# Performance work log

Hardware: AMD Instinct MI355X
Metric: run time of the kernel (lower is better)

## Reference

```python
import jax, jax.numpy as jnp
import numpy as np

B, L, E, H, RR, BIO, NT, V, R = 16, 128, 256, 256, 128, 64, 3, 30000, 25


def setup_inputs() -> dict:
    key = jax.random.key(0)
    ks = jax.random.split(key, 24)
    s = 0.05
    n = jax.random.normal
    inp = {
        'tokens': jax.random.randint(ks[0], (B, L), 0, V),
        'bio_gold': jax.random.randint(ks[1], (B, L), 0, NT),
        'selection_gold': jax.random.uniform(ks[2], (B, L, R, L), jnp.float32),
        'word_emb': n(ks[3], (V, E), jnp.float32) * s,
        'W_ih_f': n(ks[4], (4 * H, E), jnp.float32) * s,
        'W_hh_f': n(ks[5], (4 * H, H), jnp.float32) * s,
        'b_f': n(ks[6], (4 * H,), jnp.float32) * s,
        'W_ih_b': n(ks[7], (4 * H, E), jnp.float32) * s,
        'W_hh_b': n(ks[8], (4 * H, H), jnp.float32) * s,
        'b_b': n(ks[9], (4 * H,), jnp.float32) * s,
        'emi_W': n(ks[10], (NT, H), jnp.float32) * s,
        'emi_b': n(ks[11], (NT,), jnp.float32) * s,
        'bio_emb': n(ks[12], (NT + 1, BIO), jnp.float32) * s,
        'sel_u_W': n(ks[13], (RR, H + BIO), jnp.float32) * s,
        'sel_u_b': n(ks[14], (RR,), jnp.float32) * s,
        'sel_v_W': n(ks[15], (RR, H + BIO), jnp.float32) * s,
        'sel_v_b': n(ks[16], (RR,), jnp.float32) * s,
        'sel_uv_W': n(ks[17], (RR, 2 * RR), jnp.float32) * s,
        'sel_uv_b': n(ks[18], (RR,), jnp.float32) * s,
        'rel_emb': n(ks[19], (R, RR), jnp.float32) * s,
        'crf_start': n(ks[20], (NT,), jnp.float32) * s,
        'crf_end': n(ks[21], (NT,), jnp.float32) * s,
        'crf_trans': n(ks[22], (NT, NT), jnp.float32) * s,
    }
    return inp


def _lstm(x, W_ih, W_hh, b, reverse):
    # x: [B,L,E] -> hidden states [B,L,H]; PyTorch gate order i,f,g,o
    Bb = x.shape[0]
    Hh = W_hh.shape[1]
    xg = jnp.swapaxes(jnp.einsum('ble,ge->blg', x, W_ih) + b, 0, 1)  # [L,B,4H]

    def step(carry, xt):
        h, c = carry
        g = xt + h @ W_hh.T
        i, f, gg, o = jnp.split(g, 4, axis=-1)
        c = jax.nn.sigmoid(f) * c + jax.nn.sigmoid(i) * jnp.tanh(gg)
        h = jax.nn.sigmoid(o) * jnp.tanh(c)
        return (h, c), h

    init = (jnp.zeros((Bb, Hh), x.dtype), jnp.zeros((Bb, Hh), x.dtype))
    _, hs = jax.lax.scan(step, init, xg, reverse=reverse)
    return jnp.swapaxes(hs, 0, 1)


def reference(tokens, bio_gold, selection_gold, word_emb, W_ih_f, W_hh_f, b_f,
              W_ih_b, W_hh_b, b_b, emi_W, emi_b, bio_emb, sel_u_W, sel_u_b,
              sel_v_W, sel_v_b, sel_uv_W, sel_uv_b, rel_emb, crf_start,
              crf_end, crf_trans):
    mask = tokens != 0  # pad id 0
    maskf = mask.astype(jnp.float32)
    emb = word_emb[tokens]
    # BiLSTM, halves averaged as in (fwd + bwd) / 2
    o = (_lstm(emb, W_ih_f, W_hh_f, b_f, False)
         + _lstm(emb, W_ih_b, W_hh_b, b_b, True)) * 0.5
    emi = o @ emi_W.T + emi_b  # [B,L,NT]

    # ---- CRF negative log-likelihood (torchcrf, reduction='mean') ----
    bidx = jnp.arange(tokens.shape[0])
    e_sel = jnp.take_along_axis(emi, bio_gold[..., None], axis=2)[..., 0]  # [B,L]
    num = crf_start[bio_gold[:, 0]] + e_sel[:, 0]
    tr = crf_trans[bio_gold[:, :-1], bio_gold[:, 1:]]  # [B,L-1]
    num = num + ((tr + e_sel[:, 1:]) * maskf[:, 1:]).sum(1)
    seq_ends = jnp.maximum(mask.sum(1) - 1, 0)
    num = num + crf_end[bio_gold[bidx, seq_ends]]

    def crf_step(score, inp):
        emi_t, m_t = inp
        nxt = jax.nn.logsumexp(score[:, :, None] + crf_trans[None] + emi_t[:, None, :], axis=1)
        return jnp.where(m_t[:, None], nxt, score), None

    score0 = crf_start + emi[:, 0]
    score, _ = jax.lax.scan(crf_step, score0,
                            (jnp.swapaxes(emi[:, 1:], 0, 1), jnp.swapaxes(mask[:, 1:], 0, 1)))
    den = jax.nn.logsumexp(score + crf_end, axis=1)
    crf_loss = -(num - den).mean()

    # ---- pairwise biaffine selection head ----
    oc = jnp.concatenate([o, bio_emb[bio_gold]], axis=-1)  # [B,L,H+BIO]
    u = jax.nn.relu(oc @ sel_u_W.T + sel_u_b)  # [B,L,RR]
    v = jax.nn.relu(oc @ sel_v_W.T + sel_v_b)
    Rr = rel_emb.shape[1]
    W1, W2 = sel_uv_W[:, :Rr], sel_uv_W[:, Rr:]  # split cat([u,v]) linear
    a = u @ W1.T  # indexed by j (u was expanded along dim 1)
    c = v @ W2.T  # indexed by i
    uv = jax.nn.relu(a[:, None, :, :] + c[:, :, None, :] + sel_uv_b)  # [B,L,L,RR]
    logits = jnp.einsum('bijh,rh->birj', uv, rel_emb)  # [B,L,R,L]

    y = selection_gold
    bce = jnp.maximum(logits, 0) - logits * y + jnp.log1p(jnp.exp(-jnp.abs(logits)))
    selmask = maskf[:, :, None, None] * maskf[:, None, None, :]  # [B,L,1,L]
    sel_loss = (bce * selmask).sum() / maskf.sum()
    return crf_loss + sel_loss
```

## Files before the change

kernel.cpp:

```cpp
#include <hip/hip_runtime.h>
#include <cstdint>
#include <cstddef>


typedef __attribute__((ext_vector_type(8))) short short8;
typedef __attribute__((ext_vector_type(8))) int i32x8;
typedef __attribute__((ext_vector_type(4))) float f32x4;

__device__ __forceinline__ unsigned short f2bf(float f) {
  unsigned int u = __float_as_uint(f);
  u += 0x7fffu + ((u >> 16) & 1u);
  return (unsigned short)(u >> 16);
}
__device__ __forceinline__ float bf2f(unsigned short u) {
  return __uint_as_float(((unsigned int)u) << 16);
}

__device__ __forceinline__ void dev_pp8k128(const float* __restrict__ W,
                                            unsigned int* __restrict__ out, int idx) {
  int c = idx & 3;
  int lane = (idx >> 2) & 63;
  int f = idx >> 8;
  int nt = f >> 1, kt = f & 1;
  int n = nt * 16 + (lane & 15);
  int k0 = kt * 128 + (lane >> 4) * 32 + c * 8;
  const float* wp = &W[(size_t)n * 256 + k0];
  int lo = 0, hi = 0;
  lo = __builtin_amdgcn_cvt_pk_fp8_f32(wp[0], wp[1], lo, false);
  lo = __builtin_amdgcn_cvt_pk_fp8_f32(wp[2], wp[3], lo, true);
  hi = __builtin_amdgcn_cvt_pk_fp8_f32(wp[4], wp[5], hi, false);
  hi = __builtin_amdgcn_cvt_pk_fp8_f32(wp[6], wp[7], hi, true);
  size_t base = ((size_t)(f << 6) + lane) * 8 + (c << 1);
  out[base] = (unsigned)lo;
  out[base + 1] = (unsigned)hi;
}

__device__ __forceinline__ void dev_ppw(const float* __restrict__ W, int ldw, int nkt,
                                        uint4* __restrict__ out, int idx) {
  int lane = idx & 63;
  int f = idx >> 6;
  int kt = f % nkt;
  int nt = f / nkt;
  int row = nt * 16 + (lane & 15);
  int k0 = kt * 32 + ((lane >> 4) << 3);
  const float* wp = &W[(size_t)row * ldw + k0];
  union { unsigned short us[8]; uint4 v; } tmp;
#pragma unroll
  for (int j = 0; j < 8; ++j) tmp.us[j] = f2bf(wp[j]);
  out[idx] = tmp.v;
}

__global__ __launch_bounds__(256) void k_setup(
    const float* __restrict__ Whhf, unsigned int* __restrict__ wpk8f,
    const float* __restrict__ Whhb, unsigned int* __restrict__ wpk8b,
    const float* __restrict__ Wihf, uint4* __restrict__ wihfPk,
    const float* __restrict__ Wihb, uint4* __restrict__ wihbPk,
    const float* __restrict__ suW, uint4* __restrict__ suPk,
    const float* __restrict__ svW, uint4* __restrict__ svPk,
    const float* __restrict__ suvW, uint4* __restrict__ w1Pk, uint4* __restrict__ w2Pk,
    float* __restrict__ acc) {
  int bid = blockIdx.x;
  int t = threadIdx.x;
  if (bid < 128) {
    dev_pp8k128(Whhf, wpk8f, bid * 256 + t);
  } else if (bid < 256) {
    dev_pp8k128(Whhb, wpk8b, (bid - 128) * 256 + t);
  } else if (bid < 384) {
    dev_ppw(Wihf, 256, 8, wihfPk, (bid - 256) * 256 + t);
  } else if (bid < 512) {
    dev_ppw(Wihb, 256, 8, wihbPk, (bid - 384) * 256 + t);
  } else if (bid < 532) {
    dev_ppw(suW, 320, 10, suPk, (bid - 512) * 256 + t);
  } else if (bid < 552) {
    dev_ppw(svW, 320, 10, svPk, (bid - 532) * 256 + t);
  } else if (bid < 560) {
    dev_ppw(suvW, 256, 4, w1Pk, (bid - 552) * 256 + t);
  } else if (bid < 568) {
    dev_ppw(suvW + 128, 256, 4, w2Pk, (bid - 560) * 256 + t);
  } else {
    if (t < 16) acc[t] = 0.f;
  }
}

__global__ __launch_bounds__(256) void k_xg(
    const int* __restrict__ tok, const float* __restrict__ wemb,
    const uint4* __restrict__ WpkF, const float* __restrict__ biasF,
    unsigned short* __restrict__ PF,
    const uint4* __restrict__ WpkB, const float* __restrict__ biasB,
    unsigned short* __restrict__ PB) {
  const uint4* Wp = blockIdx.z ? WpkB : WpkF;
  const float* bi = blockIdx.z ? biasB : biasF;
  unsigned short* Po = blockIdx.z ? PB : PF;
  int bn = blockIdx.x, bm = blockIdx.y;
  int tid = threadIdx.x;
  int w = tid >> 6;
  int lane = tid & 63;
  int m = lane & 15;
  int q = lane >> 4;
  int arow = bm * 64 + w * 16 + m;
  const float* ew = wemb + (size_t)tok[arow] * 256 + (q << 3);
  f32x4 z = {0.f, 0.f, 0.f, 0.f};
  f32x4 ac[4] = {z, z, z, z};
  for (int kt = 0; kt < 8; ++kt) {
    float4 e0 = *reinterpret_cast<const float4*>(ew + (kt << 5));
    float4 e1 = *reinterpret_cast<const float4*>(ew + (kt << 5) + 4);
    union { unsigned short us[8]; short8 v; } af;
    af.us[0] = f2bf(e0.x); af.us[1] = f2bf(e0.y); af.us[2] = f2bf(e0.z); af.us[3] = f2bf(e0.w);
    af.us[4] = f2bf(e1.x); af.us[5] = f2bf(e1.y); af.us[6] = f2bf(e1.z); af.us[7] = f2bf(e1.w);
#pragma unroll
    for (int nt = 0; nt < 4; ++nt) {
      uint4 b4 = Wp[(size_t)(((bn << 2) + nt) * 8 + kt) * 64 + lane];
      ac[nt] = __builtin_amdgcn_mfma_f32_16x16x32_bf16(af.v, __builtin_bit_cast(short8, b4), ac[nt], 0, 0, 0);
    }
  }
#pragma unroll
  for (int nt = 0; nt < 4; ++nt) {
    int col = (bn << 6) + (nt << 4) + m;
    float bv = bi[col];
    int g = col >> 8;
    int cell = col & 255;
    int wl = cell >> 5;
    int nn = (cell >> 4) & 1;
    int mm = cell & 15;
#pragma unroll
    for (int reg = 0; reg < 4; ++reg) {
      int row = (bm << 6) + (w << 4) + (q << 2) + reg;
      int b = row >> 7;
      int t = row & 127;
      size_t pidx = ((size_t)b << 17) +
                    (size_t)(((t << 7) + (wl << 4) + mm) << 3) + (g << 1) + nn;
      Po[pidx] = f2bf(ac[nt][reg] + bv);
    }
  }
}

__global__ __launch_bounds__(512, 2) void k_lstm(
    const unsigned short* __restrict__ Pf, const unsigned short* __restrict__ Pb,
    const unsigned int* __restrict__ wpkf, const unsigned int* __restrict__ wpkb,
    unsigned short* __restrict__ hsf, unsigned short* __restrict__ hsb) {
  int bid = blockIdx.x;
  int dir = bid >> 4;
  int b = bid & 15;
  const unsigned short* P = (dir ? Pb : Pf) + ((size_t)b << 17);
  const unsigned int* wpk = dir ? wpkb : wpkf;
  unsigned short* hseq = (dir ? hsb : hsf) + (size_t)b * 128 * 256;

  __shared__ __align__(16) unsigned char h8[2][272];

  int tid = threadIdx.x;
  int w = tid >> 6;
  int lane = tid & 63;
  int m = lane & 15;
  int q = lane >> 4;
  int j0 = (w << 5) + m;

  i32x8 wfr[4][2][2];
#pragma unroll
  for (int g = 0; g < 4; ++g)
#pragma unroll
    for (int n = 0; n < 2; ++n)
#pragma unroll
      for (int kt = 0; kt < 2; ++kt) {
        int f = (((g << 4) + (w << 1) + n) << 1) + kt;
        wfr[g][n][kt] = *reinterpret_cast<const i32x8*>(wpk + (((size_t)(f << 6) + lane) << 3));
      }
#pragma unroll
  for (int g = 0; g < 4; ++g)
#pragma unroll
    for (int n = 0; n < 2; ++n)
#pragma unroll
      for (int kt = 0; kt < 2; ++kt)
        asm volatile("" : "+v"(wfr[g][n][kt]));

  if (tid < 136) reinterpret_cast<unsigned int*>(&h8[0][0])[tid] = 0u;
  __syncthreads();

  const f32x4 zero4 = {0.f, 0.f, 0.f, 0.f};
  float cst[2] = {0.f, 0.f};

  auto load_x = [&](int s) -> uint4 {
    int t = dir ? (127 - (s & 127)) : (s & 127);
    return *reinterpret_cast<const uint4*>(
        P + ((size_t)((t << 7) + (w << 4) + m) << 3));
  };

  auto step = [&](int s, uint4 x4) {
    int t = dir ? (127 - s) : s;
    const unsigned char* cur = &h8[s & 1][0];
    unsigned char* nxt = &h8[(s & 1) ^ 1][0];

    i32x8 afr[2];
#pragma unroll
    for (int kt = 0; kt < 2; ++kt) {
      union { uint4 u[2]; i32x8 v; } tmp;
      const unsigned char* hp = cur + kt * 128 + q * 32;
      tmp.u[0] = *reinterpret_cast<const uint4*>(hp);
      tmp.u[1] = *reinterpret_cast<const uint4*>(hp + 16);
      afr[kt] = tmp.v;
    }

    f32x4 acg[4][2];
    __builtin_amdgcn_s_setprio(1);
#pragma unroll
    for (int n = 0; n < 2; ++n) {
#pragma unroll
      for (int g = 0; g < 4; ++g)
        acg[g][n] = __builtin_amdgcn_mfma_scale_f32_16x16x128_f8f6f4(
            afr[0], wfr[g][n][0], zero4, 0, 0, 0, 0x7f7f7f7f, 0, 0x7f7f7f7f);
#pragma unroll
      for (int g = 0; g < 4; ++g)
        acg[g][n] = __builtin_amdgcn_mfma_scale_f32_16x16x128_f8f6f4(
            afr[1], wfr[g][n][1], acg[g][n], 0, 0, 0, 0x7f7f7f7f, 0, 0x7f7f7f7f);
    }
    __builtin_amdgcn_s_setprio(0);

    if (q == 0) {
      unsigned ug[4] = {x4.x, x4.y, x4.z, x4.w};
#pragma unroll
      for (int n = 0; n < 2; ++n) {
        float x0 = n ? __uint_as_float(ug[0] & 0xffff0000u) : __uint_as_float(ug[0] << 16);
        float x1 = n ? __uint_as_float(ug[1] & 0xffff0000u) : __uint_as_float(ug[1] << 16);
        float x2 = n ? __uint_as_float(ug[2] & 0xffff0000u) : __uint_as_float(ug[2] << 16);
        float x3 = n ? __uint_as_float(ug[3] & 0xffff0000u) : __uint_as_float(ug[3] << 16);
        float gi = acg[0][n][0] + x0;
        float gf = acg[1][n][0] + x1;
        float gg = acg[2][n][0] + x2;
        float go = acg[3][n][0] + x3;
        float si = __fdividef(1.f, 1.f + __expf(-gi));
        float sf = __fdividef(1.f, 1.f + __expf(-gf));
        float so = __fdividef(1.f, 1.f + __expf(-go));
        float tg = 1.f - __fdividef(2.f, __expf(2.f * gg) + 1.f);
        float cc = sf * cst[n] + si * tg;
        cst[n] = cc;
        float th = 1.f - __fdividef(2.f, __expf(2.f * cc) + 1.f);
        float h = so * th;
        int j = j0 + (n << 4);
        hseq[(size_t)t * 256 + j] = f2bf(h);
        int pk = __builtin_amdgcn_cvt_pk_fp8_f32(h, h, 0, false);
        nxt[j] = (unsigned char)(pk & 0xff);
      }
    }
    asm volatile("s_waitcnt lgkmcnt(0)" ::: "memory");
    __builtin_amdgcn_s_barrier();
    asm volatile("" ::: "memory");
  };

  uint4 xA = load_x(0);
  for (int sp = 0; sp < 128; sp += 2) {
    uint4 xB = load_x(sp + 1);
    step(sp, xA);
    xA = load_x(sp + 2);
    step(sp + 1, xB);
  }
}

__global__ __launch_bounds__(256) void k_mid2(
    const unsigned short* __restrict__ hf16, const unsigned short* __restrict__ hb16,
    const int* __restrict__ bio, const float* __restrict__ bioE,
    const float* __restrict__ emiW, const float* __restrict__ emib,
    const uint4* __restrict__ suPk, const float* __restrict__ sub,
    const uint4* __restrict__ svPk, const float* __restrict__ svb,
    const uint4* __restrict__ w1Pk, const uint4* __restrict__ w2Pk,
    unsigned short* __restrict__ a16, unsigned short* __restrict__ c16,
    float* __restrict__ emi) {
  __shared__ __align__(16) unsigned short oc[16][328];
  __shared__ __align__(16) unsigned short ub[16][136];
  __shared__ __align__(16) unsigned short vb[16][136];
  int r0 = blockIdx.x * 16;
  int tid = threadIdx.x;

#pragma unroll
  for (int it = 0; it < 8; ++it) {
    int i = it * 256 + tid;
    int row = i >> 7, h2 = (i & 127) << 1;
    unsigned int af = *reinterpret_cast<const unsigned int*>(hf16 + (size_t)(r0 + row) * 256 + h2);
    unsigned int ab = *reinterpret_cast<const unsigned int*>(hb16 + (size_t)(r0 + row) * 256 + h2);
    float lo = 0.5f * (bf2f((unsigned short)af) + bf2f((unsigned short)ab));
    float hi = 0.5f * (bf2f((unsigned short)(af >> 16)) + bf2f((unsigned short)(ab >> 16)));
    unsigned int pk = (unsigned int)f2bf(lo) | ((unsigned int)f2bf(hi) << 16);
    *reinterpret_cast<unsigned int*>(&oc[row][h2]) = pk;
  }
#pragma unroll
  for (int it = 0; it < 2; ++it) {
    int i = it * 256 + tid;
    int row = i >> 5, p = (i & 31) << 1;
    int bi = bio[r0 + row];
    float b0 = bioE[bi * 64 + p], b1 = bioE[bi * 64 + p + 1];
    unsigned int pk = (unsigned int)f2bf(b0) | ((unsigned int)f2bf(b1) << 16);
    *reinterpret_cast<unsigned int*>(&oc[row][256 + p]) = pk;
  }
  __syncthreads();

  if (tid < 192) {
    int did = tid >> 2, sub4 = tid & 3;
    int row = did / 3, g = did - row * 3;
    const float* ew = emiW + g * 256 + sub4 * 64;
    float av = 0.f;
#pragma unroll
    for (int k = 0; k < 64; ++k) av += bf2f(oc[row][sub4 * 64 + k]) * ew[k];
    av += __shfl_xor(av, 1);
    av += __shfl_xor(av, 2);
    if (sub4 == 0) emi[(size_t)(r0 + row) * 3 + g] = av + emib[g];
  }

  int w = tid >> 6, lane = tid & 63, m = lane & 15, q = lane >> 4;
  {
    f32x4 z = {0.f, 0.f, 0.f, 0.f};
    f32x4 au[2] = {z, z}, av2[2] = {z, z};
    for (int kt = 0; kt < 10; ++kt) {
      uint4 a4 = *reinterpret_cast<const uint4*>(&oc[m][(kt << 5) + (q << 3)]);
      short8 af = __builtin_bit_cast(short8, a4);
#pragma unroll
      for (int d = 0; d < 2; ++d) {
        int nt = (w << 1) + d;
        uint4 bu = suPk[(size_t)(nt * 10 + kt) * 64 + lane];
        uint4 bv = svPk[(size_t)(nt * 10 + kt) * 64 + lane];
        au[d] = __builtin_amdgcn_mfma_f32_16x16x32_bf16(af, __builtin_bit_cast(short8, bu), au[d], 0, 0, 0);
        av2[d] = __builtin_amdgcn_mfma_f32_16x16x32_bf16(af, __builtin_bit_cast(short8, bv), av2[d], 0, 0, 0);
      }
    }
#pragma unroll
    for (int d = 0; d < 2; ++d) {
      int col = ((w << 1) + d) * 16 + m;
      float bu = sub[col], bv = svb[col];
#pragma unroll
      for (int reg = 0; reg < 4; ++reg) {
        int row = (q << 2) + reg;
        ub[row][col] = f2bf(fmaxf(au[d][reg] + bu, 0.f));
        vb[row][col] = f2bf(fmaxf(av2[d][reg] + bv, 0.f));
      }
    }
  }
  __syncthreads();

  {
    f32x4 z = {0.f, 0.f, 0.f, 0.f};
    f32x4 aa[2] = {z, z}, cc[2] = {z, z};
    for (int kt = 0; kt < 4; ++kt) {
      uint4 ua = *reinterpret_cast<const uint4*>(&ub[m][(kt << 5) + (q << 3)]);
      uint4 va = *reinterpret_cast<const uint4*>(&vb[m][(kt << 5) + (q << 3)]);
      short8 uf = __builtin_bit_cast(short8, ua);
      short8 vf = __builtin_bit_cast(short8, va);
#pragma unroll
      for (int d = 0; d < 2; ++d) {
        int nt = (w << 1) + d;
        uint4 b1 = w1Pk[(size_t)((nt << 2) + kt) * 64 + lane];
        uint4 b2 = w2Pk[(size_t)((nt << 2) + kt) * 64 + lane];
        aa[d] = __builtin_amdgcn_mfma_f32_16x16x32_bf16(uf, __builtin_bit_cast(short8, b1), aa[d], 0, 0, 0);
        cc[d] = __builtin_amdgcn_mfma_f32_16x16x32_bf16(vf, __builtin_bit_cast(short8, b2), cc[d], 0, 0, 0);
      }
    }
#pragma unroll
    for (int d = 0; d < 2; ++d) {
      int col = ((w << 1) + d) * 16 + m;
#pragma unroll
      for (int reg = 0; reg < 4; ++reg) {
        int row = r0 + (q << 2) + reg;
        a16[(size_t)row * 128 + col] = f2bf(aa[d][reg]);
        c16[(size_t)row * 128 + col] = f2bf(cc[d][reg]);
      }
    }
  }
}

__global__ __launch_bounds__(256) void k_loss(
    const unsigned short* __restrict__ a16, const unsigned short* __restrict__ c16,
    const float* __restrict__ suvb, const float* __restrict__ rel,
    const float* __restrict__ y, const int* __restrict__ tok,
    const float* __restrict__ emi, const int* __restrict__ bio,
    const float* __restrict__ cstart, const float* __restrict__ cend,
    const float* __restrict__ ctrans,
    float* __restrict__ acc, float* __restrict__ out) {
  int blk = blockIdx.x;
  int tid = threadIdx.x;
  if (blk < 1024) {
    __shared__ unsigned short alds[128][136];
    __shared__ float cbs[2][128];
    __shared__ float red[4];
    int b = blk >> 6;
    int ip = blk & 63;
    int hh = tid & 127;
    int half = tid >> 7;
#pragma unroll
    for (int it = 0; it < 32; ++it) {
      int idx = it * 256 + tid;
      int jrow = idx >> 6;
      int h2 = (idx & 63) << 1;
      unsigned int av = *reinterpret_cast<const unsigned int*>(
          a16 + ((size_t)(b << 7) + jrow) * 128 + h2);
      alds[h2][jrow] = (unsigned short)av;
      alds[h2 + 1][jrow] = (unsigned short)(av >> 16);
    }
    {
      int i = (ip << 1) + half;
      cbs[half][hh] = bf2f(c16[(size_t)((b << 7) + i) * 128 + hh]) + suvb[hh];
    }
    __syncthreads();
    int i = (ip << 1) + half;
    int j = hh;
    float lg[25];
#pragma unroll
    for (int r = 0; r < 25; ++r) lg[r] = 0.f;
    for (int h = 0; h < 128; ++h) {
      float av = bf2f(alds[h][j]);
      float uv = fmaxf(av + cbs[half][h], 0.f);
#pragma unroll
      for (int r = 0; r < 25; ++r) lg[r] += uv * rel[r * 128 + h];
    }
    float mi = (tok[(b << 7) + i] != 0) ? 1.f : 0.f;
    float mj = (tok[(b << 7) + j] != 0) ? 1.f : 0.f;
    const float* yp = y + (size_t)((b << 7) + i) * 3200 + j;
    float bs = 0.f;
#pragma unroll
    for (int r = 0; r < 25; ++r) {
      float x = lg[r];
      float yv = yp[r * 128];
      bs += fmaxf(x, 0.f) - x * yv + __logf(1.f + __expf(-fabsf(x)));
    }
    bs *= mi * mj;
#pragma unroll
    for (int off = 32; off; off >>= 1) bs += __shfl_down(bs, off);
    if ((tid & 63) == 0) red[tid >> 6] = bs;
    __syncthreads();
    if (tid == 0) atomicAdd(&acc[0], red[0] + red[1] + red[2] + red[3]);
  } else {
    __shared__ float elds[128][4];
    __shared__ float msk[128];
    __shared__ int biol[128];
    __shared__ float r_t[2], r_m[2];
    int b = blk - 1024;
    int t = tid;
    if (t < 128) {
      biol[t] = bio[b * 128 + t];
      msk[t] = (tok[b * 128 + t] != 0) ? 1.f : 0.f;
#pragma unroll
      for (int g = 0; g < 3; ++g) elds[t][g] = emi[(b * 128 + t) * 3 + g];
    }
    __syncthreads();
    if (t < 128) {
      float m = msk[t];
      float term;
      if (t == 0)
        term = cstart[biol[0]] + elds[0][biol[0]];
      else
        term = (ctrans[biol[t - 1] * 3 + biol[t]] + elds[t][biol[t]]) * m;
      float ms = m;
#pragma unroll
      for (int off = 32; off; off >>= 1) {
        term += __shfl_down(term, off);
        ms += __shfl_down(ms, off);
      }
      if ((t & 63) == 0) { r_t[t >> 6] = term; r_m[t >> 6] = ms; }
    }
    __syncthreads();
    if (t == 0) {
      float num = r_t[0] + r_t[1];
      float msum = r_m[0] + r_m[1];
      int se = (int)msum - 1;
      if (se < 0) se = 0;
      num += cend[biol[se]];
      float tr[9];
#pragma unroll
      for (int i2 = 0; i2 < 9; ++i2) tr[i2] = ctrans[i2];
      float s0 = cstart[0] + elds[0][0];
      float s1 = cstart[1] + elds[0][1];
      float s2 = cstart[2] + elds[0][2];
      for (int tt = 1; tt < 128; ++tt) {
        float a0, a1, a2, mx, n0, n1, n2;
        a0 = s0 + tr[0]; a1 = s1 + tr[3]; a2 = s2 + tr[6];
        mx = fmaxf(a0, fmaxf(a1, a2));
        n0 = mx + __logf(__expf(a0 - mx) + __expf(a1 - mx) + __expf(a2 - mx)) + elds[tt][0];
        a0 = s0 + tr[1]; a1 = s1 + tr[4]; a2 = s2 + tr[7];
        mx = fmaxf(a0, fmaxf(a1, a2));
        n1 = mx + __logf(__expf(a0 - mx) + __expf(a1 - mx) + __expf(a2 - mx)) + elds[tt][1];
        a0 = s0 + tr[2]; a1 = s1 + tr[5]; a2 = s2 + tr[8];
        mx = fmaxf(a0, fmaxf(a1, a2));
        n2 = mx + __logf(__expf(a0 - mx) + __expf(a1 - mx) + __expf(a2 - mx)) + elds[tt][2];
        if (msk[tt] != 0.f) { s0 = n0; s1 = n1; s2 = n2; }
      }
      float a0 = s0 + cend[0], a1 = s1 + cend[1], a2 = s2 + cend[2];
      float mx = fmaxf(a0, fmaxf(a1, a2));
      float den = mx + __logf(__expf(a0 - mx) + __expf(a1 - mx) + __expf(a2 - mx));
      atomicAdd(&acc[1], num - den);
      atomicAdd(&acc[2], msum);
    }
  }
  if (tid == 0) {
    __threadfence();
    unsigned old = atomicAdd((unsigned int*)(acc + 5), 1u);
    if (old == 1039u) {
      __threadfence();
      float s0 = atomicAdd(&acc[0], 0.f);
      float s1 = atomicAdd(&acc[1], 0.f);
      float s2 = atomicAdd(&acc[2], 0.f);
      out[0] = -(s1 * (1.f / 16.f)) + s0 / s2;
    }
  }
}

extern "C" void kernel_launch(void* const* d_in, const int* in_sizes, int n_in,
                              void* d_out, int out_size, void* d_ws, size_t ws_size,
                              hipStream_t stream) {
  const int* tokens = (const int*)d_in[0];
  const int* bio = (const int*)d_in[1];
  const float* selg = (const float*)d_in[2];
  const float* wemb = (const float*)d_in[3];
  const float* Wihf = (const float*)d_in[4];
  const float* Whhf = (const float*)d_in[5];
  const float* bf = (const float*)d_in[6];
  const float* Wihb = (const float*)d_in[7];
  const float* Whhb = (const float*)d_in[8];
  const float* bb = (const float*)d_in[9];
  const float* emiW = (const float*)d_in[10];
  const float* emib = (const float*)d_in[11];
  const float* bioE = (const float*)d_in[12];
  const float* suW = (const float*)d_in[13];
  const float* sub = (const float*)d_in[14];
  const float* svW = (const float*)d_in[15];
  const float* svb = (const float*)d_in[16];
  const float* suvW = (const float*)d_in[17];
  const float* suvb = (const float*)d_in[18];
  const float* rel = (const float*)d_in[19];
  const float* cstart = (const float*)d_in[20];
  const float* cend = (const float*)d_in[21];
  const float* ctrans = (const float*)d_in[22];

  float* ws = (float*)d_ws;
  float* xgf16 = ws;
  float* xgb16 = xgf16 + 1048576;
  float* hf16 = xgb16 + 1048576;
  float* hb16 = hf16 + 262144;
  float* a16 = hb16 + 262144;
  float* c16 = a16 + 131072;
  float* emi = c16 + 131072;
  float* wpk8f = emi + 6144;
  float* wpk8b = wpk8f + 65536;
  float* wihfPk = wpk8b + 65536;
  float* wihbPk = wihfPk + 131072;
  float* suPk = wihbPk + 131072;
  float* svPk = suPk + 20480;
  float* w1Pk = svPk + 20480;
  float* w2Pk = w1Pk + 8192;
  float* acc = w2Pk + 8192;

  k_setup<<<569, 256, 0, stream>>>(
      Whhf, (unsigned int*)wpk8f, Whhb, (unsigned int*)wpk8b,
      Wihf, (uint4*)wihfPk, Wihb, (uint4*)wihbPk,
      suW, (uint4*)suPk, svW, (uint4*)svPk,
      suvW, (uint4*)w1Pk, (uint4*)w2Pk, acc);

  k_xg<<<dim3(16, 32, 2), 256, 0, stream>>>(
      tokens, wemb,
      (const uint4*)wihfPk, bf, (unsigned short*)xgf16,
      (const uint4*)wihbPk, bb, (unsigned short*)xgb16);

  k_lstm<<<32, 512, 0, stream>>>(
      (const unsigned short*)xgf16, (const unsigned short*)xgb16,
      (const unsigned int*)wpk8f, (const unsigned int*)wpk8b,
      (unsigned short*)hf16, (unsigned short*)hb16);

  k_mid2<<<128, 256, 0, stream>>>(
      (const unsigned short*)hf16, (const unsigned short*)hb16,
      bio, bioE, emiW, emib,
      (const uint4*)suPk, sub, (const uint4*)svPk, svb,
      (const uint4*)w1Pk, (const uint4*)w2Pk,
      (unsigned short*)a16, (unsigned short*)c16, emi);

  k_loss<<<1040, 256, 0, stream>>>((const unsigned short*)a16, (const unsigned short*)c16,
                                   suvb, rel, selg, tokens, emi, bio,
                                   cstart, cend, ctrans, acc, (float*)d_out);
}
```

Measured before the change: 387.5 us.

## Stage xg output in LDS for coalesced stores; split LSTM gate math across quads

The input-projection kernel now has each block compute all 1024 gate columns for 16 rows. It writes results into a shared-memory tile and then stores them with coalesced 16-byte writes, replacing the scattered 2-byte global stores. In the LSTM recurrence, the two gate-output halves that one quad used to handle serially are now spread across quads 0 and 1. This shortens the serial activation chain on each step, and the setprio hints around the MFMA block are removed. The price is a 32 KB LDS tile, a block-wide sync and 16 accumulators per thread in k_xg, plus redundant activation work in quads 2 and 3.

Result: faster. 348.3 us (-10.1%).

```diff
diff --git a/kernel.cpp b/kernel.cpp
--- a/kernel.cpp
+++ b/kernel.cpp
@@ -88,19 +88,19 @@
     unsigned short* __restrict__ PF,
     const uint4* __restrict__ WpkB, const float* __restrict__ biasB,
     unsigned short* __restrict__ PB) {
-  const uint4* Wp = blockIdx.z ? WpkB : WpkF;
-  const float* bi = blockIdx.z ? biasB : biasF;
-  unsigned short* Po = blockIdx.z ? PB : PF;
-  int bn = blockIdx.x, bm = blockIdx.y;
+  const uint4* Wp = blockIdx.y ? WpkB : WpkF;
+  const float* bi = blockIdx.y ? biasB : biasF;
+  unsigned short* Po = blockIdx.y ? PB : PF;
+  __shared__ __align__(16) unsigned short oc[16][1024];
+  int r0 = blockIdx.x * 16;
   int tid = threadIdx.x;
   int w = tid >> 6;
   int lane = tid & 63;
   int m = lane & 15;
   int q = lane >> 4;
-  int arow = bm * 64 + w * 16 + m;
-  const float* ew = wemb + (size_t)tok[arow] * 256 + (q << 3);
+  const float* ew = wemb + (size_t)tok[r0 + m] * 256 + (q << 3);
   f32x4 z = {0.f, 0.f, 0.f, 0.f};
-  f32x4 ac[4] = {z, z, z, z};
+  f32x4 ac[16] = {z, z, z, z, z, z, z, z, z, z, z, z, z, z, z, z};
   for (int kt = 0; kt < 8; ++kt) {
     float4 e0 = *reinterpret_cast<const float4*>(ew + (kt << 5));
     float4 e1 = *reinterpret_cast<const float4*>(ew + (kt << 5) + 4);
@@ -108,29 +108,35 @@
     af.us[0] = f2bf(e0.x); af.us[1] = f2bf(e0.y); af.us[2] = f2bf(e0.z); af.us[3] = f2bf(e0.w);
     af.us[4] = f2bf(e1.x); af.us[5] = f2bf(e1.y); af.us[6] = f2bf(e1.z); af.us[7] = f2bf(e1.w);
 #pragma unroll
-    for (int nt = 0; nt < 4; ++nt) {
-      uint4 b4 = Wp[(size_t)(((bn << 2) + nt) * 8 + kt) * 64 + lane];
-      ac[nt] = __builtin_amdgcn_mfma_f32_16x16x32_bf16(af.v, __builtin_bit_cast(short8, b4), ac[nt], 0, 0, 0);
-    }
-  }
-#pragma unroll
-  for (int nt = 0; nt < 4; ++nt) {
-    int col = (bn << 6) + (nt << 4) + m;
+    for (int j = 0; j < 16; ++j) {
+      int nt = (w << 4) + j;
+      uint4 b4 = Wp[(size_t)(nt * 8 + kt) * 64 + lane];
+      ac[j] = __builtin_amdgcn_mfma_f32_16x16x32_bf16(af.v, __builtin_bit_cast(short8, b4), ac[j], 0, 0, 0);
+    }
+  }
+#pragma unroll
+  for (int j = 0; j < 16; ++j) {
+    int col = (w << 8) + (j << 4) + m;
     float bv = bi[col];
-    int g = col >> 8;
-    int cell = col & 255;
-    int wl = cell >> 5;
-    int nn = (cell >> 4) & 1;
-    int mm = cell & 15;
+    int cellp = ((j >> 1) << 4) | m;
+    int sub = (w << 1) | (j & 1);
 #pragma unroll
     for (int reg = 0; reg < 4; ++reg) {
-      int row = (bm << 6) + (w << 4) + (q << 2) + reg;
-      int b = row >> 7;
-      int t = row & 127;
-      size_t pidx = ((size_t)b << 17) +
-                    (size_t)(((t << 7) + (wl << 4) + mm) << 3) + (g << 1) + nn;
-      Po[pidx] = f2bf(ac[nt][reg] + bv);
-    }
+      int row = (q << 2) + reg;
+      oc[row][(cellp << 3) + sub] = f2bf(ac[j][reg] + bv);
+    }
+  }
+  __syncthreads();
+  int b = r0 >> 7;
+  unsigned short* Pb = Po + ((size_t)b << 17);
+#pragma unroll
+  for (int i = 0; i < 8; ++i) {
+    int idx = i * 256 + tid;
+    int row = idx >> 7;
+    int c8 = idx & 127;
+    uint4 v = *reinterpret_cast<const uint4*>(&oc[row][c8 << 3]);
+    int t = (r0 + row) & 127;
+    *reinterpret_cast<uint4*>(Pb + ((size_t)t << 10) + (c8 << 3)) = v;
   }
 }
 
@@ -152,7 +158,8 @@
   int lane = tid & 63;
   int m = lane & 15;
   int q = lane >> 4;
-  int j0 = (w << 5) + m;
+  int nsel = q & 1;
+  int jj = (w << 5) + m + (nsel << 4);
 
   i32x8 wfr[4][2][2];
 #pragma unroll
@@ -176,7 +183,7 @@
   __syncthreads();
 
   const f32x4 zero4 = {0.f, 0.f, 0.f, 0.f};
-  float cst[2] = {0.f, 0.f};
+  float cst = 0.f;
 
   auto load_x = [&](int s) -> uint4 {
     int t = dir ? (127 - (s & 127)) : (s & 127);
@@ -200,7 +207,6 @@
     }
 
     f32x4 acg[4][2];
-    __builtin_amdgcn_s_setprio(1);
 #pragma unroll
     for (int n = 0; n < 2; ++n) {
 #pragma unroll
@@ -212,32 +218,29 @@
         acg[g][n] = __builtin_amdgcn_mfma_scale_f32_16x16x128_f8f6f4(
             afr[1], wfr[g][n][1], acg[g][n], 0, 0, 0, 0x7f7f7f7f, 0, 0x7f7f7f7f);
     }
-    __builtin_amdgcn_s_setprio(0);
-
-    if (q == 0) {
-      unsigned ug[4] = {x4.x, x4.y, x4.z, x4.w};
-#pragma unroll
-      for (int n = 0; n < 2; ++n) {
-        float x0 = n ? __uint_as_float(ug[0] & 0xffff0000u) : __uint_as_float(ug[0] << 16);
-        float x1 = n ? __uint_as_float(ug[1] & 0xffff0000u) : __uint_as_float(ug[1] << 16);
-        float x2 = n ? __uint_as_float(ug[2] & 0xffff0000u) : __uint_as_float(ug[2] << 16);
-        float x3 = n ? __uint_as_float(ug[3] & 0xffff0000u) : __uint_as_float(ug[3] << 16);
-        float gi = acg[0][n][0] + x0;
-        float gf = acg[1][n][0] + x1;
-        float gg = acg[2][n][0] + x2;
-        float go = acg[3][n][0] + x3;
-        float si = __fdividef(1.f, 1.f + __expf(-gi));
-        float sf = __fdividef(1.f, 1.f + __expf(-gf));
-        float so = __fdividef(1.f, 1.f + __expf(-go));
-        float tg = 1.f - __fdividef(2.f, __expf(2.f * gg) + 1.f);
-        float cc = sf * cst[n] + si * tg;
-        cst[n] = cc;
-        float th = 1.f - __fdividef(2.f, __expf(2.f * cc) + 1.f);
-        float h = so * th;
-        int j = j0 + (n << 4);
-        hseq[(size_t)t * 256 + j] = f2bf(h);
+
+    {
+      unsigned u0 = x4.x, u1 = x4.y, u2 = x4.z, u3 = x4.w;
+      float x0 = __uint_as_float(nsel ? (u0 & 0xffff0000u) : (u0 << 16));
+      float x1 = __uint_as_float(nsel ? (u1 & 0xffff0000u) : (u1 << 16));
+      float x2 = __uint_as_float(nsel ? (u2 & 0xffff0000u) : (u2 << 16));
+      float x3 = __uint_as_float(nsel ? (u3 & 0xffff0000u) : (u3 << 16));
+      float gi = (nsel ? acg[0][1][0] : acg[0][0][0]) + x0;
+      float gf = (nsel ? acg[1][1][0] : acg[1][0][0]) + x1;
+      float gg = (nsel ? acg[2][1][0] : acg[2][0][0]) + x2;
+      float go = (nsel ? acg[3][1][0] : acg[3][0][0]) + x3;
+      float si = __fdividef(1.f, 1.f + __expf(-gi));
+      float sf = __fdividef(1.f, 1.f + __expf(-gf));
+      float so = __fdividef(1.f, 1.f + __expf(-go));
+      float tg = 1.f - __fdividef(2.f, __expf(2.f * gg) + 1.f);
+      float cc = sf * cst + si * tg;
+      cst = cc;
+      float th = 1.f - __fdividef(2.f, __expf(2.f * cc) + 1.f);
+      float h = so * th;
+      if (q < 2) {
+        hseq[(size_t)t * 256 + jj] = f2bf(h);
         int pk = __builtin_amdgcn_cvt_pk_fp8_f32(h, h, 0, false);
-        nxt[j] = (unsigned char)(pk & 0xff);
+        nxt[jj] = (unsigned char)(pk & 0xff);
       }
     }
     asm volatile("s_waitcnt lgkmcnt(0)" ::: "memory");
@@ -549,7 +552,7 @@
       suW, (uint4*)suPk, svW, (uint4*)svPk,
       suvW, (uint4*)w1Pk, (uint4*)w2Pk, acc);
 
-  k_xg<<<dim3(16, 32, 2), 256, 0, stream>>>(
+  k_xg<<<dim3(128, 2), 256, 0, stream>>>(
       tokens, wemb,
       (const uint4*)wihfPk, bf, (unsigned short*)xgf16,
       (const uint4*)wihbPk, bb, (unsigned short*)xgb16);
```
